# Performance work log

Hardware: AMD Instinct MI355X
Metric: run time of the kernel (lower is better)

## Reference

```python
import jax, jax.numpy as jnp
import numpy as np

CONF_THRES = 0.596
IOU_THRES = 0.45
CELL_LIMIT = 200   # CELL_SIZE_LIMIT
MAX_CAND = 512     # fixed candidate pool for jit-able NMS
MAX_WH = 4096.0    # per-class NMS box offset (yolov5 trick)
NEG_SLOPE = 0.01   # LeakyReLU default


def xywh2xyxy(b):
    cx, cy, w, h = b[..., 0], b[..., 1], b[..., 2], b[..., 3]
    return jnp.stack([cx - w / 2, cy - h / 2, cx + w / 2, cy + h / 2], axis=-1)


def box_iou(a, b):
    # a:[N,4] b:[M,4] xyxy -> [N,M]
    area_a = (a[:, 2] - a[:, 0]) * (a[:, 3] - a[:, 1])
    area_b = (b[:, 2] - b[:, 0]) * (b[:, 3] - b[:, 1])
    lt = jnp.maximum(a[:, None, :2], b[None, :, :2])
    rb = jnp.minimum(a[:, None, 2:], b[None, :, 2:])
    wh = jnp.clip(rb - lt, 0.0)
    inter = wh[..., 0] * wh[..., 1]
    return inter / (area_a[:, None] + area_b[None, :] - inter + 1e-9)


def nms_single(pred):
    # pred [N,85]: xywh, obj, 80 class probs (yolov5 layout)
    obj = pred[:, 4]
    conf_cls = pred[:, 5:] * obj[:, None]
    conf = conf_cls.max(-1)
    cls = jnp.argmax(conf_cls, -1).astype(jnp.float32)
    box = xywh2xyxy(pred[:, :4])
    score = jnp.where(conf > CONF_THRES, conf, -1.0)
    order = jnp.argsort(-score)[:MAX_CAND]          # top candidates, score-sorted
    boxes, scores, cls = box[order], score[order], cls[order]
    off = boxes + cls[:, None] * MAX_WH             # per-class offset
    iou = box_iou(off, off)
    idx = jnp.arange(MAX_CAND)
    def body(i, keep):
        sup = (iou[i] > IOU_THRES) & (idx > i) & keep[i]
        return keep & ~sup
    keep = jax.lax.fori_loop(0, MAX_CAND, body, scores > 0.0)  # greedy NMS
    ks = jnp.where(keep, scores, -1.0)
    top = jnp.argsort(-ks)[:CELL_LIMIT]
    return boxes[top], ks[top] > 0.0                # [200,4], [200]


def roi_align_1x1(feat, boxes, scale):
    # feat [C,H,W]; boxes [M,4] xyxy image pixels; output_size=1, 2x2 bilinear samples
    C, H, W = feat.shape
    b = boxes * scale
    x1, y1 = b[:, 0], b[:, 1]
    bw = jnp.maximum(b[:, 2] - x1, 1.0)
    bh = jnp.maximum(b[:, 3] - y1, 1.0)
    g = jnp.array([0.25, 0.75], dtype=feat.dtype)   # (i+0.5)/2 sample offsets
    xs = x1[:, None] + g[None, :] * bw[:, None]     # [M,2]
    ys = y1[:, None] + g[None, :] * bh[:, None]
    X = jnp.tile(xs, (1, 2))                        # [M,4] x varies fast
    Y = jnp.repeat(ys, 2, axis=1)
    X = jnp.clip(X, 0.0, W - 1.0)
    Y = jnp.clip(Y, 0.0, H - 1.0)
    x0 = jnp.floor(X).astype(jnp.int32); y0 = jnp.floor(Y).astype(jnp.int32)
    x1i = jnp.minimum(x0 + 1, W - 1); y1i = jnp.minimum(y0 + 1, H - 1)
    wx = X - x0; wy = Y - y0
    v = (feat[:, y0, x0] * ((1 - wy) * (1 - wx))[None]
         + feat[:, y0, x1i] * ((1 - wy) * wx)[None]
         + feat[:, y1i, x0] * (wy * (1 - wx))[None]
         + feat[:, y1i, x1i] * (wy * wx)[None])     # [C,M,4]
    return v.mean(-1).T                             # [M,C]


def reference(out, x1, x2, x3, x4, W1, b1, W2, b2):
    Himg = x1.shape[-2] * 8
    Wimg = x1.shape[-1] * 8
    whwh = jnp.array([Wimg, Himg, Wimg, Himg], dtype=jnp.float32)
    boxes, mask = jax.vmap(nms_single)(out)         # [B,200,4], [B,200]

    def per_img(f1, f2, f3, f4, bb):
        r = jnp.concatenate([
            roi_align_1x1(f1, bb, 1 / 8),
            roi_align_1x1(f2, bb, 1 / 16),
            roi_align_1x1(f3, bb, 1 / 32),
            roi_align_1x1(f4, bb, 1 / 64)], axis=-1)          # [200,1920]
        h = jax.nn.leaky_relu(r @ W1 + b1, NEG_SLOPE)
        h = jax.nn.leaky_relu(h @ W2 + b2, NEG_SLOPE)
        return jnp.concatenate([bb / whwh, h], axis=-1)        # [200,68]

    feats = jax.vmap(per_img)(x1, x2, x3, x4, boxes)
    feats = feats * mask[..., None].astype(feats.dtype)       # zero padded rows
    return feats, mask


def setup_inputs() -> dict:
    key = jax.random.key(0)
    ks = jax.random.split(key, 10)
    B, IMG = 8, 1024
    N = ((IMG // 8) ** 2 + (IMG // 16) ** 2 + (IMG // 32) ** 2) * 3  # 64512
    cxcy = jax.random.uniform(ks[0], (B, N, 2)) * IMG
    wh = jax.random.uniform(ks[1], (B, N, 2)) * 240.0 + 16.0
    obj = jax.random.uniform(ks[2], (B, N, 1))
    cls = jax.random.uniform(ks[3], (B, N, 80))
    out = jnp.concatenate([cxcy, wh, obj, cls], axis=-1)
    x1 = jax.random.normal(ks[4], (B, 128, 128, 128), dtype=jnp.float32)
    x2 = jax.random.normal(ks[5], (B, 256, 64, 64), dtype=jnp.float32)
    x3 = jax.random.normal(ks[6], (B, 512, 32, 32), dtype=jnp.float32)
    x4 = jax.random.normal(ks[7], (B, 1024, 16, 16), dtype=jnp.float32)
    W1 = jax.random.normal(ks[8], (1920, 64)) * 0.02
    b1 = jnp.zeros((64,), jnp.float32)
    W2 = jax.random.normal(ks[9], (64, 64)) * 0.1
    b2 = jnp.zeros((64,), jnp.float32)
    return dict(out=out, x1=x1, x2=x2, x3=x3, x4=x4, W1=W1, b1=b1, W2=W2, b2=b2)
```

## Files before the change

kernel.cpp:

```cpp
#include <hip/hip_runtime.h>
#include <hip/hip_bf16.h>

typedef unsigned int u32;
typedef unsigned long long u64;
typedef unsigned char u8;

#define B_IMG 8
#define N_ANCH 64512
#define NCLS 80
#define ROW 85
#define CONF_T 0.596f
#define IOU_T 0.45f
#define MAXC 512
#define CELL 200
#define CAP 4096

#define HBKT 128
#define KEYBASE 0x3F18u

#define SR 96
#define SF4 ((SR * ROW) / 4)
#define TOT_F4 ((size_t)B_IMG * N_ANCH * ROW / 4)

__device__ __forceinline__ float fsub(float a, float b){ return __fsub_rn(a,b); }
__device__ __forceinline__ float fadd(float a, float b){ return __fadd_rn(a,b); }
__device__ __forceinline__ float fmul(float a, float b){ return __fmul_rn(a,b); }

__device__ __forceinline__ u64 shfl_u64(u64 v, int src) {
    u32 lo = (u32)(v & 0xFFFFFFFFull), hi = (u32)(v >> 32);
    lo = (u32)__shfl((int)lo, src);
    hi = (u32)__shfl((int)hi, src);
    return ((u64)hi << 32) | (u64)lo;
}

__global__ __launch_bounds__(256) void k_score(const float* __restrict__ outp,
                                               float* __restrict__ scores,
                                               u8* __restrict__ clsarr,
                                               u32* __restrict__ hist) {
    __shared__ float srows[SR * ROW];

    int tid = threadIdx.x;
    size_t base = (size_t)blockIdx.x * SF4;
    const float4* src = (const float4*)outp;

    size_t a = base + tid;
    const size_t amax = TOT_F4 - 1;
    float4 t0 = src[(a            < amax) ? (a           ) : amax];
    float4 t1 = src[(a + 256      < amax) ? (a + 256     ) : amax];
    float4 t2 = src[(a + 512      < amax) ? (a + 512     ) : amax];
    float4 t3 = src[(a + 768      < amax) ? (a + 768     ) : amax];
    float4 t4 = src[(a + 1024     < amax) ? (a + 1024    ) : amax];
    float4 t5 = src[(a + 1280     < amax) ? (a + 1280    ) : amax];
    float4 t6 = src[(a + 1536     < amax) ? (a + 1536    ) : amax];
    float4 t7 = src[(a + 1792     < amax) ? (a + 1792    ) : amax];

    float4* dst = (float4*)srows;
    dst[tid        ] = t0;
    dst[tid +  256 ] = t1;
    dst[tid +  512 ] = t2;
    dst[tid +  768 ] = t3;
    dst[tid + 1024 ] = t4;
    dst[tid + 1280 ] = t5;
    dst[tid + 1536 ] = t6;
    if (tid < SF4 - 1792) dst[tid + 1792] = t7;
    __syncthreads();

    int r = tid >> 1;
    int h = tid & 1;
    float score = -1.0f;
    int cls = 0;
    int gi = blockIdx.x * SR + r;
    if (tid < 192) {
        const float* row = srows + r * ROW;
        float obj = row[4];
        const float* cp = row + 5 + h * 40;
        float best = -1.0f; int bi = h * 40;
        #pragma unroll
        for (int c = 0; c < 40; ++c) {
            float v = fmul(cp[c], obj);
            if (v > best) { best = v; bi = h * 40 + c; }
        }
        float ob  = __shfl_xor(best, 1);
        int   obi = __shfl_xor(bi, 1);
        float conf;
        if (ob > best) { conf = ob; cls = obi; }
        else           { conf = best; cls = bi; }
        score = (conf > CONF_T) ? conf : -1.0f;
    }

    if (tid < 192 && h == 0) {
        scores[gi] = score;
        clsarr[gi] = (u8)cls;
        if (score > 0.0f) {
            int b = gi / N_ANCH;
            u32 bk = (__float_as_uint(score) >> 16) - KEYBASE;
            if (bk > HBKT - 1) bk = HBKT - 1;
            atomicAdd(&hist[(size_t)b * HBKT + bk], 1u);
        }
    }
}

__global__ __launch_bounds__(128) void k_thresh(const u32* __restrict__ hist,
                                                u32* __restrict__ thresh) {
    int b = blockIdx.x;
    int tid = threadIdx.x;
    __shared__ u32 h[HBKT];
    h[tid] = hist[(size_t)b * HBKT + tid];
    __syncthreads();
    if (tid == 0) {
        u32 c2 = 0;
        int bkt = HBKT - 1;
        for (; bkt >= 0; --bkt) {
            c2 += h[bkt];
            if (c2 >= MAXC) break;
        }
        thresh[b] = (bkt < 0) ? 0u : (((u32)bkt + KEYBASE) << 16);
    }
}

__global__ __launch_bounds__(256) void k_compact(const float* __restrict__ scores,
                                                 const u32* __restrict__ thresh,
                                                 u32* __restrict__ cnt,
                                                 u64* __restrict__ list) {
    int i = blockIdx.x * blockDim.x + threadIdx.x;
    if (i >= B_IMG * N_ANCH) return;
    float s = scores[i];
    if (s <= 0.0f) return;
    int b = i / N_ANCH;
    u32 key = __float_as_uint(s);
    if (key < thresh[b]) return;
    u32 pos = atomicAdd(&cnt[b], 1u);
    if (pos < CAP) {
        u32 n = (u32)(i - b * N_ANCH);
        list[(size_t)b * CAP + pos] = ((u64)key << 32) | (u64)(0xFFFFFFFFu - n);
    }
}

__global__ __launch_bounds__(512) void k_sort(const float* __restrict__ outp,
                                              const u8* __restrict__ clsarr,
                                              const u32* __restrict__ cnt,
                                              const u64* __restrict__ list,
                                              float* __restrict__ oboxw,
                                              float* __restrict__ areaw,
                                              float* __restrict__ bxw,
                                              u32* __restrict__ nvalidw) {
    __shared__ u64 buf[CAP];
    int b = blockIdx.x;
    int tid = threadIdx.x;

    int M = (int)min(cnt[b], (u32)CAP);
    int P = MAXC;
    while (P < M) P <<= 1;

    for (int t = tid; t < P; t += 512)
        buf[t] = (t < M) ? list[(size_t)b * CAP + t] : 0ull;
    __syncthreads();

    for (int k = 2; k <= P; k <<= 1) {
        for (int j = k >> 1; j > 0; j >>= 1) {
            for (int t = tid; t < P; t += 512) {
                int ixj = t ^ j;
                if (ixj > t) {
                    u64 a = buf[t], c = buf[ixj];
                    bool desc = ((t & k) == 0);
                    if (desc ? (a < c) : (a > c)) { buf[t] = c; buf[ixj] = a; }
                }
            }
            __syncthreads();
        }
    }

    int nvalid = min(M, MAXC);
    bool valid = (tid < nvalid);
    u32 n = 0;
    if (valid) n = 0xFFFFFFFFu - (u32)(buf[tid] & 0xFFFFFFFFull);

    float bx0, bx1, bx2, bx3;
    float ob0, ob1, ob2, ob3;
    if (valid) {
        const float* p = outp + ((size_t)b * N_ANCH + n) * ROW;
        float cx = p[0], cy = p[1], w = p[2], h = p[3];
        int bi = (int)clsarr[(size_t)b * N_ANCH + n];
        float hw = fmul(w, 0.5f), hh = fmul(h, 0.5f);
        bx0 = fsub(cx, hw); bx1 = fsub(cy, hh);
        bx2 = fadd(cx, hw); bx3 = fadd(cy, hh);
        float off = fmul((float)bi, 4096.0f);
        ob0 = fadd(bx0, off); ob1 = fadd(bx1, off);
        ob2 = fadd(bx2, off); ob3 = fadd(bx3, off);
    } else {
        bx0 = bx1 = bx2 = bx3 = 0.0f;
        ob0 = ob1 = ob2 = ob3 = -1.0e6f;
    }
    ((float4*)oboxw)[b * MAXC + tid] = make_float4(ob0, ob1, ob2, ob3);
    areaw[b * MAXC + tid] = fmul(fsub(ob2, ob0), fsub(ob3, ob1));
    ((float4*)bxw)[b * MAXC + tid] = make_float4(bx0, bx1, bx2, bx3);
    if (tid == 0) nvalidw[b] = (u32)nvalid;
}

__global__ __launch_bounds__(64) void k_iou(const float* __restrict__ oboxw,
                                            const float* __restrict__ areaw,
                                            u64* __restrict__ sup) {
    int t = blockIdx.x, b = blockIdx.y;
    int ti = 0;
    while (t >= 8 - ti) { t -= 8 - ti; ++ti; }
    int tj = ti + t;

    int lane = threadIdx.x;
    int i = ti * 64 + lane;
    float4 oi = ((const float4*)oboxw)[b * MAXC + i];
    float ai = areaw[b * MAXC + i];

    __shared__ float jb[5][64];
    int jg = tj * 64 + lane;
    float4 oj = ((const float4*)oboxw)[b * MAXC + jg];
    jb[0][lane] = oj.x; jb[1][lane] = oj.y;
    jb[2][lane] = oj.z; jb[3][lane] = oj.w;
    jb[4][lane] = areaw[b * MAXC + jg];
    __syncthreads();

    u64 bits = 0;
    for (int jl = 0; jl < 64; ++jl) {
        int j = tj * 64 + jl;
        float ltx = fmaxf(oi.x, jb[0][jl]);
        float lty = fmaxf(oi.y, jb[1][jl]);
        float rbx = fminf(oi.z, jb[2][jl]);
        float rby = fminf(oi.w, jb[3][jl]);
        float ww = fmaxf(fsub(rbx, ltx), 0.0f);
        float hh2 = fmaxf(fsub(rby, lty), 0.0f);
        float inter = fmul(ww, hh2);
        float denom = fadd(fsub(fadd(ai, jb[4][jl]), inter), 1e-9f);
        float iou = __fdiv_rn(inter, denom);
        if ((j > i) && (iou > IOU_T)) bits |= (1ull << jl);
    }

    u64* sr = sup + ((size_t)(b * MAXC + i)) * 8;
    if (ti == tj) {
        for (int w = 0; w < ti; ++w) sr[w] = 0ull;
    }
    sr[tj] = bits;
}

#define GW(W, KW, NE, APPLY) \
    { u64 todo = (KW) & (NE); \
      while (todo) { \
          int bb = (int)__builtin_ctzll(todo); \
          const u64* rr = srow + (((W) * 64 + bb) * 8); \
          u64 hm = (bb < 63) ? (~0ull << (bb + 1)) : 0ull; \
          KW &= ~(rr[W] & hm); \
          APPLY \
          todo &= hm & KW; \
      } }

__global__ __launch_bounds__(512) void k_greedy(const u64* __restrict__ sup,
                                                const u32* __restrict__ nvalidw,
                                                const float* __restrict__ bxw,
                                                float* __restrict__ selbox,
                                                u32* __restrict__ selcnt,
                                                float* __restrict__ mask_out) {
    __shared__ u64 srow[MAXC * 8];
    __shared__ u64 neword[8];
    __shared__ u64 keepw[8];
    int b = blockIdx.x;
    int tid = threadIdx.x;
    int nvalid = (int)nvalidw[b];

    const u64* g = sup + (size_t)b * MAXC * 8;
    u64 r0 = g[tid*8+0], r1 = g[tid*8+1], r2 = g[tid*8+2], r3 = g[tid*8+3];
    u64 r4 = g[tid*8+4], r5 = g[tid*8+5], r6 = g[tid*8+6], r7 = g[tid*8+7];
    srow[tid*8+0]=r0; srow[tid*8+1]=r1; srow[tid*8+2]=r2; srow[tid*8+3]=r3;
    srow[tid*8+4]=r4; srow[tid*8+5]=r5; srow[tid*8+6]=r6; srow[tid*8+7]=r7;
    bool ne = ((r0|r1|r2|r3|r4|r5|r6|r7) != 0ull);
    u64 bal = __ballot(ne);
    if ((tid & 63) == 0) neword[tid >> 6] = bal;
    if (tid < 8) {
        int lo = tid * 64;
        u64 kw = 0;
        if (nvalid >= lo + 64) kw = ~0ull;
        else if (nvalid > lo) kw = (1ull << (nvalid - lo)) - 1ull;
        keepw[tid] = kw;
    }
    __syncthreads();

    if (tid == 0) {
        u64 k0=keepw[0], k1=keepw[1], k2=keepw[2], k3=keepw[3];
        u64 k4=keepw[4], k5=keepw[5], k6=keepw[6], k7=keepw[7];
        u64 n0=neword[0], n1=neword[1], n2=neword[2], n3=neword[3];
        u64 n4=neword[4], n5=neword[5], n6=neword[6], n7=neword[7];
        GW(0, k0, n0, k1&=~rr[1]; k2&=~rr[2]; k3&=~rr[3]; k4&=~rr[4]; k5&=~rr[5]; k6&=~rr[6]; k7&=~rr[7];)
        GW(1, k1, n1, k2&=~rr[2]; k3&=~rr[3]; k4&=~rr[4]; k5&=~rr[5]; k6&=~rr[6]; k7&=~rr[7];)
        GW(2, k2, n2, k3&=~rr[3]; k4&=~rr[4]; k5&=~rr[5]; k6&=~rr[6]; k7&=~rr[7];)
        GW(3, k3, n3, k4&=~rr[4]; k5&=~rr[5]; k6&=~rr[6]; k7&=~rr[7];)
        GW(4, k4, n4, k5&=~rr[5]; k6&=~rr[6]; k7&=~rr[7];)
        GW(5, k5, n5, k6&=~rr[6]; k7&=~rr[7];)
        GW(6, k6, n6, k7&=~rr[7];)
        GW(7, k7, n7, )
        keepw[0]=k0; keepw[1]=k1; keepw[2]=k2; keepw[3]=k3;
        keepw[4]=k4; keepw[5]=k5; keepw[6]=k6; keepw[7]=k7;
    }
    __syncthreads();

    int w = tid >> 6, l = tid & 63;
    bool kept = (tid < nvalid) && ((keepw[w] >> l) & 1ull);
    int rank = 0;
    for (int ww = 0; ww < w; ++ww) rank += __popcll(keepw[ww]);
    rank += __popcll(keepw[w] & ((l == 0) ? 0ull : ((1ull << l) - 1ull)));
    if (kept && rank < CELL) {
        float4 bx = ((const float4*)bxw)[b * MAXC + tid];
        float* sb = selbox + ((size_t)b * CELL + rank) * 4;
        sb[0] = bx.x; sb[1] = bx.y; sb[2] = bx.z; sb[3] = bx.w;
        mask_out[b * CELL + rank] = 1.0f;
    }
    if (tid == 0) {
        int tot = 0;
        for (int ww = 0; ww < 8; ++ww) tot += __popcll(keepw[ww]);
        selcnt[b] = (u32)min(tot, CELL);
    }
}

__global__ __launch_bounds__(512) void k_nms(const float* __restrict__ outp,
                                             const u32* __restrict__ cnt,
                                             const u64* __restrict__ list,
                                             float* __restrict__ selbox,
                                             u32* __restrict__ selcnt,
                                             float* __restrict__ mask_out) {
    __shared__ u64 buf[CAP];
    __shared__ float obox[MAXC][4];
    __shared__ float area[MAXC];
    __shared__ u64 keepw[8];
    int b = blockIdx.x;
    int tid = threadIdx.x;

    int M = (int)min(cnt[b], (u32)CAP);
    int P = MAXC;
    while (P < M) P <<= 1;

    for (int t = tid; t < P; t += 512)
        buf[t] = (t < M) ? list[(size_t)b * CAP + t] : 0ull;
    __syncthreads();

    for (int k = 2; k <= P; k <<= 1) {
        for (int j = k >> 1; j > 0; j >>= 1) {
            for (int t = tid; t < P; t += 512) {
                int ixj = t ^ j;
                if (ixj > t) {
                    u64 a = buf[t], c = buf[ixj];
                    bool desc = ((t & k) == 0);
                    if (desc ? (a < c) : (a > c)) { buf[t] = c; buf[ixj] = a; }
                }
            }
            __syncthreads();
        }
    }

    int nvalid = min(M, MAXC);
    bool valid = (tid < nvalid);
    u32 n = 0;
    if (valid) n = 0xFFFFFFFFu - (u32)(buf[tid] & 0xFFFFFFFFull);
    __syncthreads();

    float bx0, bx1, bx2, bx3;
    float ob0, ob1, ob2, ob3;
    if (valid) {
        const float* p = outp + ((size_t)b * N_ANCH + n) * ROW;
        float cx = p[0], cy = p[1], w = p[2], h = p[3], obj = p[4];
        float best = -1.0f; int bi = 0;
        for (int c = 0; c < NCLS; ++c) {
            float v = fmul(p[5 + c], obj);
            if (v > best) { best = v; bi = c; }
        }
        float hw = fmul(w, 0.5f), hh = fmul(h, 0.5f);
        bx0 = fsub(cx, hw); bx1 = fsub(cy, hh);
        bx2 = fadd(cx, hw); bx3 = fadd(cy, hh);
        float off = fmul((float)bi, 4096.0f);
        ob0 = fadd(bx0, off); ob1 = fadd(bx1, off);
        ob2 = fadd(bx2, off); ob3 = fadd(bx3, off);
    } else {
        bx0 = bx1 = bx2 = bx3 = 0.0f;
        ob0 = ob1 = ob2 = ob3 = -1.0e6f;
    }
    obox[tid][0] = ob0; obox[tid][1] = ob1;
    obox[tid][2] = ob2; obox[tid][3] = ob3;
    area[tid] = fmul(fsub(ob2, ob0), fsub(ob3, ob1));
    __syncthreads();

    u64* sup = buf;
    {
        u64 rowb[8] = {0,0,0,0,0,0,0,0};
        float aa = area[tid];
        for (int j = tid + 1; j < MAXC; ++j) {
            float ltx = fmaxf(ob0, obox[j][0]);
            float lty = fmaxf(ob1, obox[j][1]);
            float rbx = fminf(ob2, obox[j][2]);
            float rby = fminf(ob3, obox[j][3]);
            float ww = fmaxf(fsub(rbx, ltx), 0.0f);
            float hh2 = fmaxf(fsub(rby, lty), 0.0f);
            float inter = fmul(ww, hh2);
            float denom = fadd(fsub(fadd(aa, area[j]), inter), 1e-9f);
            float iou = __fdiv_rn(inter, denom);
            if (iou > IOU_T) rowb[j >> 6] |= (1ull << (j & 63));
        }
        for (int w2 = 0; w2 < 8; ++w2) sup[tid * 8 + w2] = rowb[w2];
    }
    __syncthreads();

    if (tid < 64) {
        int lane = tid;
        u64 kw = 0;
        if (lane < 8) {
            int lo = lane * 64;
            if (nvalid >= lo + 64) kw = ~0ull;
            else if (nvalid > lo) kw = (1ull << (nvalid - lo)) - 1ull;
        }
        for (int i = 0; i < MAXC; ++i) {
            u64 wv = shfl_u64(kw, i >> 6);
            if ((wv >> (i & 63)) & 1ull) {
                if (lane < 8) kw &= ~sup[(size_t)i * 8 + lane];
            }
        }
        if (lane < 8) keepw[lane] = kw;
    }
    __syncthreads();

    int w = tid >> 6, l = tid & 63;
    bool kept = valid && ((keepw[w] >> l) & 1ull);
    int rank = 0;
    for (int ww = 0; ww < w; ++ww) rank += __popcll(keepw[ww]);
    rank += __popcll(keepw[w] & ((l == 0) ? 0ull : ((1ull << l) - 1ull)));
    if (kept && rank < CELL) {
        float* sb = selbox + ((size_t)b * CELL + rank) * 4;
        sb[0] = bx0; sb[1] = bx1; sb[2] = bx2; sb[3] = bx3;
        mask_out[b * CELL + rank] = 1.0f;
    }
    if (tid == 0) {
        int tot = 0;
        for (int ww = 0; ww < 8; ++ww) tot += __popcll(keepw[ww]);
        selcnt[b] = (u32)min(tot, CELL);
    }
}

__global__ __launch_bounds__(256) void k_roi_gather(
        const float* __restrict__ x1, const float* __restrict__ x2,
        const float* __restrict__ x3, const float* __restrict__ x4,
        const float* __restrict__ selbox, const u32* __restrict__ selcnt,
        float* __restrict__ rws) {
    int slot = blockIdx.y;
    int b = blockIdx.z;
    if (slot >= (int)selcnt[b]) return;

    int unit = blockIdx.x * 256 + threadIdx.x;
    int c = unit >> 2;
    int p = unit & 3;

    const float* fb; int Wd; float s; int cl;
    if (c < 128)      { fb = x1 + (size_t)b * 128 * 128 * 128; Wd = 128; s = 0.125f;    cl = c; }
    else if (c < 384) { fb = x2 + (size_t)b * 256 * 64 * 64;   Wd = 64;  s = 0.0625f;   cl = c - 128; }
    else if (c < 896) { fb = x3 + (size_t)b * 512 * 32 * 32;   Wd = 32;  s = 0.03125f;  cl = c - 384; }
    else              { fb = x4 + (size_t)b * 1024 * 16 * 16;  Wd = 16;  s = 0.015625f; cl = c - 896; }

    const float* sb = selbox + ((size_t)b * CELL + slot) * 4;
    float box0 = sb[0], box1 = sb[1], box2 = sb[2], box3 = sb[3];

    float bx1f = box0 * s, by1f = box1 * s;
    float bw = fmaxf(box2 * s - bx1f, 1.0f);
    float bh = fmaxf(box3 * s - by1f, 1.0f);
    float gx = (p & 1)  ? 0.75f : 0.25f;
    float gy = (p >> 1) ? 0.75f : 0.25f;
    float X = bx1f + gx * bw;
    float Y = by1f + gy * bh;
    X = fminf(fmaxf(X, 0.0f), (float)(Wd - 1));
    Y = fminf(fmaxf(Y, 0.0f), (float)(Wd - 1));
    int x0 = (int)floorf(X), y0 = (int)floorf(Y);
    int x1i = min(x0 + 1, Wd - 1), y1i = min(y0 + 1, Wd - 1);
    float wx = X - (float)x0, wy = Y - (float)y0;

    const float* f = fb + (size_t)cl * Wd * Wd;
    float v = f[y0 * Wd + x0]  * ((1.0f - wy) * (1.0f - wx))
            + f[y0 * Wd + x1i] * ((1.0f - wy) * wx)
            + f[y1i * Wd + x0] * (wy * (1.0f - wx))
            + f[y1i * Wd + x1i]* (wy * wx);

    int lane = threadIdx.x & 63;
    int base = lane & ~3;
    float v0 = __shfl(v, base + 0);
    float v1 = __shfl(v, base + 1);
    float v2 = __shfl(v, base + 2);
    float v3 = __shfl(v, base + 3);
    if (p == 0) {
        rws[((size_t)b * CELL + slot) * 1920 + c] = (((v0 + v1) + v2) + v3) * 0.25f;
    }
}

__global__ __launch_bounds__(256) void k_mlp(
        const float* __restrict__ W1, const float* __restrict__ b1,
        const float* __restrict__ W2, const float* __restrict__ b2,
        const float* __restrict__ selbox, const u32* __restrict__ selcnt,
        const float* __restrict__ rws, float* __restrict__ feats) {
    int slot0 = blockIdx.x * 4;
    int b = blockIdx.y;
    int nsel = (int)selcnt[b];
    if (slot0 >= nsel) return;
    int tid = threadIdx.x;

    __shared__ float psum[4][4][64];
    __shared__ float h1s[4][64];

    int j = tid & 63, part = tid >> 6;
    const float* r0 = rws + ((size_t)b * CELL + slot0 + 0) * 1920;
    const float* r1 = rws + ((size_t)b * CELL + slot0 + 1) * 1920;
    const float* r2 = rws + ((size_t)b * CELL + slot0 + 2) * 1920;
    const float* r3 = rws + ((size_t)b * CELL + slot0 + 3) * 1920;

    {
        float a0 = 0.0f, a1 = 0.0f, a2 = 0.0f, a3 = 0.0f;
        int k0 = part * 480;
        for (int k = k0; k < k0 + 480; ++k) {
            float w = W1[(size_t)k * 64 + j];
            a0 += r0[k] * w;
            a1 += r1[k] * w;
            a2 += r2[k] * w;
            a3 += r3[k] * w;
        }
        psum[0][part][j] = a0;
        psum[1][part][j] = a1;
        psum[2][part][j] = a2;
        psum[3][part][j] = a3;
    }
    __syncthreads();

    int sl = tid >> 6;
    int slot = slot0 + sl;
    if (slot < nsel) {
        float v = psum[sl][0][j] + psum[sl][1][j] + psum[sl][2][j] + psum[sl][3][j] + b1[j];
        h1s[sl][j] = (v >= 0.0f) ? v : 0.01f * v;
    }
    __syncthreads();

    if (slot < nsel) {
        float acc = b2[j];
        for (int k = 0; k < 64; ++k) acc += h1s[sl][k] * W2[k * 64 + j];
        float v = (acc >= 0.0f) ? acc : 0.01f * acc;
        float* orow = feats + ((size_t)b * CELL + slot) * 68;
        orow[4 + j] = v;
        if (j < 4) {
            const float* sb = selbox + ((size_t)b * CELL + slot) * 4;
            orow[j] = sb[j] * (1.0f / 1024.0f);
        }
    }
}

__global__ __launch_bounds__(256) void k_roi_mlp(
        const float* __restrict__ x1, const float* __restrict__ x2,
        const float* __restrict__ x3, const float* __restrict__ x4,
        const float* __restrict__ W1, const float* __restrict__ b1,
        const float* __restrict__ W2, const float* __restrict__ b2,
        const float* __restrict__ selbox, const u32* __restrict__ selcnt,
        float* __restrict__ feats) {
    int slot = blockIdx.x;
    int b = blockIdx.y;
    if (slot >= (int)selcnt[b]) return;
    int tid = threadIdx.x;

    __shared__ float r[1920];
    __shared__ float psum[4][64];
    __shared__ float h1[64];

    const float* sb = selbox + ((size_t)b * CELL + slot) * 4;
    float box0 = sb[0], box1 = sb[1], box2 = sb[2], box3 = sb[3];

    const float* feat[4] = {
        x1 + (size_t)b * 128 * 128 * 128,
        x2 + (size_t)b * 256 * 64 * 64,
        x3 + (size_t)b * 512 * 32 * 32,
        x4 + (size_t)b * 1024 * 16 * 16
    };
    const int   Cs[4]  = {128, 256, 512, 1024};
    const int   Wd_[4] = {128, 64, 32, 16};
    const float Ss[4]  = {0.125f, 0.0625f, 0.03125f, 0.015625f};
    const int   Off[4] = {0, 128, 384, 896};

    for (int lvl = 0; lvl < 4; ++lvl) {
        int Wd = Wd_[lvl], C = Cs[lvl];
        float s = Ss[lvl];
        float bx1f = box0 * s, by1f = box1 * s;
        float bw = fmaxf(box2 * s - bx1f, 1.0f);
        float bh = fmaxf(box3 * s - by1f, 1.0f);
        float xs[2] = { bx1f + 0.25f * bw, bx1f + 0.75f * bw };
        float ys[2] = { by1f + 0.25f * bh, by1f + 0.75f * bh };
        int idx[4][4]; float wt[4][4];
        for (int p = 0; p < 4; ++p) {
            float X = xs[p & 1], Y = ys[p >> 1];
            X = fminf(fmaxf(X, 0.0f), (float)(Wd - 1));
            Y = fminf(fmaxf(Y, 0.0f), (float)(Wd - 1));
            int x0 = (int)floorf(X), y0 = (int)floorf(Y);
            int x1i = min(x0 + 1, Wd - 1), y1i = min(y0 + 1, Wd - 1);
            float wx = X - (float)x0, wy = Y - (float)y0;
            idx[p][0] = y0 * Wd + x0;  idx[p][1] = y0 * Wd + x1i;
            idx[p][2] = y1i * Wd + x0; idx[p][3] = y1i * Wd + x1i;
            wt[p][0] = (1.0f - wy) * (1.0f - wx); wt[p][1] = (1.0f - wy) * wx;
            wt[p][2] = wy * (1.0f - wx);          wt[p][3] = wy * wx;
        }
        const float* fb = feat[lvl];
        int HW = Wd * Wd;
        for (int c = tid; c < C; c += 256) {
            const float* f = fb + (size_t)c * HW;
            float acc = 0.0f;
            for (int p = 0; p < 4; ++p)
                acc += f[idx[p][0]] * wt[p][0] + f[idx[p][1]] * wt[p][1]
                     + f[idx[p][2]] * wt[p][2] + f[idx[p][3]] * wt[p][3];
            r[Off[lvl] + c] = acc * 0.25f;
        }
    }
    __syncthreads();

    int j = tid & 63, part = tid >> 6;
    {
        float acc = 0.0f;
        int k0 = part * 480;
        for (int k = k0; k < k0 + 480; ++k)
            acc += r[k] * W1[(size_t)k * 64 + j];
        psum[part][j] = acc;
    }
    __syncthreads();
    if (tid < 64) {
        float v = psum[0][tid] + psum[1][tid] + psum[2][tid] + psum[3][tid] + b1[tid];
        h1[tid] = (v >= 0.0f) ? v : 0.01f * v;
    }
    __syncthreads();

    float* orow = feats + ((size_t)b * CELL + slot) * 68;
    if (tid < 64) {
        float acc = b2[tid];
        for (int k = 0; k < 64; ++k) acc += h1[k] * W2[k * 64 + tid];
        float v = (acc >= 0.0f) ? acc : 0.01f * acc;
        orow[4 + tid] = v;
    }
    if (tid < 4) {
        float bv = (tid == 0) ? box0 : (tid == 1) ? box1 : (tid == 2) ? box2 : box3;
        orow[tid] = bv * (1.0f / 1024.0f);
    }
}

extern "C" void kernel_launch(void* const* d_in, const int* in_sizes, int n_in,
                              void* d_out, int out_size, void* d_ws, size_t ws_size,
                              hipStream_t stream) {
    const float* outp = (const float*)d_in[0];
    const float* x1 = (const float*)d_in[1];
    const float* x2 = (const float*)d_in[2];
    const float* x3 = (const float*)d_in[3];
    const float* x4 = (const float*)d_in[4];
    const float* W1 = (const float*)d_in[5];
    const float* b1 = (const float*)d_in[6];
    const float* W2 = (const float*)d_in[7];
    const float* b2 = (const float*)d_in[8];

    char* ws = (char*)d_ws;
    const size_t o_cnt    = 0;
    const size_t o_hist   = 256;
    const size_t o_thresh = 4352;
    const size_t o_scores = 4608;
    const size_t o_cls    = o_scores + 2064384;
    const size_t o_list   = o_cls + 516096;
    const size_t o_selbox = o_list + 262144;
    const size_t o_selcnt = o_selbox + 25600;
    const size_t o_rws    = o_selcnt + 256;
    const size_t ws_need_rws = o_rws + (size_t)B_IMG * CELL * 1920 * 4;
    const size_t o_sup    = ws_need_rws;
    const size_t o_obox   = o_sup + 262144;
    const size_t o_area   = o_obox + 65536;
    const size_t o_bx     = o_area + 16384;
    const size_t o_nvalid = o_bx + 65536;
    const size_t ws_need_full = o_nvalid + 256;

    u32*   cnt    = (u32*)(ws + o_cnt);
    u32*   hist   = (u32*)(ws + o_hist);
    u32*   thresh = (u32*)(ws + o_thresh);
    float* scores = (float*)(ws + o_scores);
    u8*    clsarr = (u8*)(ws + o_cls);
    u64*   list   = (u64*)(ws + o_list);
    float* selbox = (float*)(ws + o_selbox);
    u32*   selcnt = (u32*)(ws + o_selcnt);
    float* rws    = (float*)(ws + o_rws);
    u64*   sup    = (u64*)(ws + o_sup);
    float* oboxw  = (float*)(ws + o_obox);
    float* areaw  = (float*)(ws + o_area);
    float* bxw    = (float*)(ws + o_bx);
    u32*   nvalidw= (u32*)(ws + o_nvalid);

    float* feats = (float*)d_out;
    float* mask  = feats + (size_t)B_IMG * CELL * 68;

    hipMemsetAsync(d_out, 0, (size_t)out_size * sizeof(float), stream);
    hipMemsetAsync(ws, 0, 4608, stream);

    int total = B_IMG * N_ANCH;
    int blocks = (total + 255) / 256;
    int score_blocks = total / SR;
    k_score  <<<score_blocks, 256, 0, stream>>>(outp, scores, clsarr, hist);
    k_thresh <<<B_IMG, 128, 0, stream>>>(hist, thresh);
    k_compact<<<blocks, 256, 0, stream>>>(scores, thresh, cnt, list);

    if (ws_size >= ws_need_full) {
        k_sort  <<<B_IMG, 512, 0, stream>>>(outp, clsarr, cnt, list, oboxw, areaw, bxw, nvalidw);
        k_iou   <<<dim3(36, B_IMG), 64, 0, stream>>>(oboxw, areaw, sup);
        k_greedy<<<B_IMG, 512, 0, stream>>>(sup, nvalidw, bxw, selbox, selcnt, mask);
    } else {
        k_nms   <<<B_IMG, 512, 0, stream>>>(outp, cnt, list, selbox, selcnt, mask);
    }

    if (ws_size >= ws_need_rws) {
        k_roi_gather<<<dim3(30, CELL, B_IMG), 256, 0, stream>>>(
            x1, x2, x3, x4, selbox, selcnt, rws);
        k_mlp<<<dim3((CELL + 3) / 4, B_IMG), 256, 0, stream>>>(
            W1, b1, W2, b2, selbox, selcnt, rws, feats);
    } else {
        k_roi_mlp<<<dim3(CELL, B_IMG), 256, 0, stream>>>(
            x1, x2, x3, x4, W1, b1, W2, b2, selbox, selcnt, feats);
    }
}
```

Baseline: 343.0 us.

## Fuse threshold into compaction and merge sort, IoU, greedy NMS into one kernel

```diff
diff --git a/kernel.cpp b/kernel.cpp
--- a/kernel.cpp
+++ b/kernel.cpp
@@ -22,16 +22,11 @@
 #define SF4 ((SR * ROW) / 4)
 #define TOT_F4 ((size_t)B_IMG * N_ANCH * ROW / 4)
 
+#define BLK_PER_IMG (N_ANCH / 256)
+
 __device__ __forceinline__ float fsub(float a, float b){ return __fsub_rn(a,b); }
 __device__ __forceinline__ float fadd(float a, float b){ return __fadd_rn(a,b); }
 __device__ __forceinline__ float fmul(float a, float b){ return __fmul_rn(a,b); }
-
-__device__ __forceinline__ u64 shfl_u64(u64 v, int src) {
-    u32 lo = (u32)(v & 0xFFFFFFFFull), hi = (u32)(v >> 32);
-    lo = (u32)__shfl((int)lo, src);
-    hi = (u32)__shfl((int)hi, src);
-    return ((u64)hi << 32) | (u64)lo;
-}
 
 __global__ __launch_bounds__(256) void k_score(const float* __restrict__ outp,
                                                float* __restrict__ scores,
@@ -100,12 +95,15 @@
     }
 }
 
-__global__ __launch_bounds__(128) void k_thresh(const u32* __restrict__ hist,
-                                                u32* __restrict__ thresh) {
-    int b = blockIdx.x;
+__global__ __launch_bounds__(256) void k_compact(const float* __restrict__ scores,
+                                                 const u32* __restrict__ hist,
+                                                 u32* __restrict__ cnt,
+                                                 u64* __restrict__ list) {
+    __shared__ u32 h[HBKT];
+    __shared__ u32 sthresh;
+    int b = blockIdx.x / BLK_PER_IMG;
     int tid = threadIdx.x;
-    __shared__ u32 h[HBKT];
-    h[tid] = hist[(size_t)b * HBKT + tid];
+    if (tid < HBKT) h[tid] = hist[(size_t)b * HBKT + tid];
     __syncthreads();
     if (tid == 0) {
         u32 c2 = 0;
@@ -114,21 +112,15 @@
             c2 += h[bkt];
             if (c2 >= MAXC) break;
         }
-        thresh[b] = (bkt < 0) ? 0u : (((u32)bkt + KEYBASE) << 16);
-    }
-}
-
-__global__ __launch_bounds__(256) void k_compact(const float* __restrict__ scores,
-                                                 const u32* __restrict__ thresh,
-                                                 u32* __restrict__ cnt,
-                                                 u64* __restrict__ list) {
-    int i = blockIdx.x * blockDim.x + threadIdx.x;
-    if (i >= B_IMG * N_ANCH) return;
+        sthresh = (bkt < 0) ? 0u : (((u32)bkt + KEYBASE) << 16);
+    }
+    __syncthreads();
+
+    int i = blockIdx.x * 256 + tid;
     float s = scores[i];
     if (s <= 0.0f) return;
-    int b = i / N_ANCH;
     u32 key = __float_as_uint(s);
-    if (key < thresh[b]) return;
+    if (key < sthresh) return;
     u32 pos = atomicAdd(&cnt[b], 1u);
     if (pos < CAP) {
         u32 n = (u32)(i - b * N_ANCH);
@@ -136,15 +128,30 @@
     }
 }
 
-__global__ __launch_bounds__(512) void k_sort(const float* __restrict__ outp,
+#define GW(W, KW, NE, APPLY) \
+    { u64 todo = (KW) & (NE); \
+      while (todo) { \
+          int bb = (int)__builtin_ctzll(todo); \
+          const u64* rr = srow + (((W) * 64 + bb) * 8); \
+          u64 hm = (bb < 63) ? (~0ull << (bb + 1)) : 0ull; \
+          KW &= ~(rr[W] & hm); \
+          APPLY \
+          todo &= hm & KW; \
+      } }
+
+__global__ __launch_bounds__(512) void k_nms2(const float* __restrict__ outp,
                                               const u8* __restrict__ clsarr,
                                               const u32* __restrict__ cnt,
                                               const u64* __restrict__ list,
-                                              float* __restrict__ oboxw,
-                                              float* __restrict__ areaw,
-                                              float* __restrict__ bxw,
-                                              u32* __restrict__ nvalidw) {
+                                              float* __restrict__ selbox,
+                                              u32* __restrict__ selcnt,
+                                              float* __restrict__ mask_out) {
     __shared__ u64 buf[CAP];
+    __shared__ float4 oboxs[MAXC];
+    __shared__ float  areas[MAXC];
+    __shared__ float4 bxs[MAXC];
+    __shared__ u64 keepw[8];
+    __shared__ u64 neword[8];
     int b = blockIdx.x;
     int tid = threadIdx.x;
 
@@ -174,6 +181,7 @@
     bool valid = (tid < nvalid);
     u32 n = 0;
     if (valid) n = 0xFFFFFFFFu - (u32)(buf[tid] & 0xFFFFFFFFull);
+    __syncthreads();
 
     float bx0, bx1, bx2, bx3;
     float ob0, ob1, ob2, ob3;
@@ -191,87 +199,53 @@
         bx0 = bx1 = bx2 = bx3 = 0.0f;
         ob0 = ob1 = ob2 = ob3 = -1.0e6f;
     }
-    ((float4*)oboxw)[b * MAXC + tid] = make_float4(ob0, ob1, ob2, ob3);
-    areaw[b * MAXC + tid] = fmul(fsub(ob2, ob0), fsub(ob3, ob1));
-    ((float4*)bxw)[b * MAXC + tid] = make_float4(bx0, bx1, bx2, bx3);
-    if (tid == 0) nvalidw[b] = (u32)nvalid;
-}
-
-__global__ __launch_bounds__(64) void k_iou(const float* __restrict__ oboxw,
-                                            const float* __restrict__ areaw,
-                                            u64* __restrict__ sup) {
-    int t = blockIdx.x, b = blockIdx.y;
-    int ti = 0;
-    while (t >= 8 - ti) { t -= 8 - ti; ++ti; }
-    int tj = ti + t;
-
-    int lane = threadIdx.x;
-    int i = ti * 64 + lane;
-    float4 oi = ((const float4*)oboxw)[b * MAXC + i];
-    float ai = areaw[b * MAXC + i];
-
-    __shared__ float jb[5][64];
-    int jg = tj * 64 + lane;
-    float4 oj = ((const float4*)oboxw)[b * MAXC + jg];
-    jb[0][lane] = oj.x; jb[1][lane] = oj.y;
-    jb[2][lane] = oj.z; jb[3][lane] = oj.w;
-    jb[4][lane] = areaw[b * MAXC + jg];
-    __syncthreads();
-
-    u64 bits = 0;
-    for (int jl = 0; jl < 64; ++jl) {
-        int j = tj * 64 + jl;
-        float ltx = fmaxf(oi.x, jb[0][jl]);
-        float lty = fmaxf(oi.y, jb[1][jl]);
-        float rbx = fminf(oi.z, jb[2][jl]);
-        float rby = fminf(oi.w, jb[3][jl]);
-        float ww = fmaxf(fsub(rbx, ltx), 0.0f);
-        float hh2 = fmaxf(fsub(rby, lty), 0.0f);
-        float inter = fmul(ww, hh2);
-        float denom = fadd(fsub(fadd(ai, jb[4][jl]), inter), 1e-9f);
-        float iou = __fdiv_rn(inter, denom);
-        if ((j > i) && (iou > IOU_T)) bits |= (1ull << jl);
-    }
-
-    u64* sr = sup + ((size_t)(b * MAXC + i)) * 8;
-    if (ti == tj) {
-        for (int w = 0; w < ti; ++w) sr[w] = 0ull;
-    }
-    sr[tj] = bits;
-}
-
-#define GW(W, KW, NE, APPLY) \
-    { u64 todo = (KW) & (NE); \
-      while (todo) { \
-          int bb = (int)__builtin_ctzll(todo); \
-          const u64* rr = srow + (((W) * 64 + bb) * 8); \
-          u64 hm = (bb < 63) ? (~0ull << (bb + 1)) : 0ull; \
-          KW &= ~(rr[W] & hm); \
-          APPLY \
-          todo &= hm & KW; \
-      } }
-
-__global__ __launch_bounds__(512) void k_greedy(const u64* __restrict__ sup,
-                                                const u32* __restrict__ nvalidw,
-                                                const float* __restrict__ bxw,
-                                                float* __restrict__ selbox,
-                                                u32* __restrict__ selcnt,
-                                                float* __restrict__ mask_out) {
-    __shared__ u64 srow[MAXC * 8];
-    __shared__ u64 neword[8];
-    __shared__ u64 keepw[8];
-    int b = blockIdx.x;
-    int tid = threadIdx.x;
-    int nvalid = (int)nvalidw[b];
-
-    const u64* g = sup + (size_t)b * MAXC * 8;
-    u64 r0 = g[tid*8+0], r1 = g[tid*8+1], r2 = g[tid*8+2], r3 = g[tid*8+3];
-    u64 r4 = g[tid*8+4], r5 = g[tid*8+5], r6 = g[tid*8+6], r7 = g[tid*8+7];
-    srow[tid*8+0]=r0; srow[tid*8+1]=r1; srow[tid*8+2]=r2; srow[tid*8+3]=r3;
-    srow[tid*8+4]=r4; srow[tid*8+5]=r5; srow[tid*8+6]=r6; srow[tid*8+7]=r7;
-    bool ne = ((r0|r1|r2|r3|r4|r5|r6|r7) != 0ull);
-    u64 bal = __ballot(ne);
-    if ((tid & 63) == 0) neword[tid >> 6] = bal;
+    oboxs[tid] = make_float4(ob0, ob1, ob2, ob3);
+    areas[tid] = fmul(fsub(ob2, ob0), fsub(ob3, ob1));
+    bxs[tid]   = make_float4(bx0, bx1, bx2, bx3);
+    __syncthreads();
+
+    u64* sup = buf;
+    {
+        int wave = tid >> 6, lane = tid & 63;
+        for (int t = wave; t < 36; t += 8) {
+            int tt = t, ti = 0;
+            while (tt >= 8 - ti) { tt -= 8 - ti; ++ti; }
+            int tj = ti + tt;
+
+            int i = ti * 64 + lane;
+            float4 oi = oboxs[i];
+            float ai = areas[i];
+            u64 bits = 0;
+            for (int jl = 0; jl < 64; ++jl) {
+                int j = tj * 64 + jl;
+                float4 oj = oboxs[j];
+                float aj = areas[j];
+                float ltx = fmaxf(oi.x, oj.x);
+                float lty = fmaxf(oi.y, oj.y);
+                float rbx = fminf(oi.z, oj.z);
+                float rby = fminf(oi.w, oj.w);
+                float ww = fmaxf(fsub(rbx, ltx), 0.0f);
+                float hh2 = fmaxf(fsub(rby, lty), 0.0f);
+                float inter = fmul(ww, hh2);
+                float denom = fadd(fsub(fadd(ai, aj), inter), 1e-9f);
+                float iou = __fdiv_rn(inter, denom);
+                if ((j > i) && (iou > IOU_T)) bits |= (1ull << jl);
+            }
+            if (ti == tj) {
+                for (int w = 0; w < ti; ++w) sup[(size_t)i * 8 + w] = 0ull;
+            }
+            sup[(size_t)i * 8 + tj] = bits;
+        }
+    }
+    __syncthreads();
+
+    {
+        u64 r0 = sup[tid*8+0], r1 = sup[tid*8+1], r2 = sup[tid*8+2], r3 = sup[tid*8+3];
+        u64 r4 = sup[tid*8+4], r5 = sup[tid*8+5], r6 = sup[tid*8+6], r7 = sup[tid*8+7];
+        bool ne = ((r0|r1|r2|r3|r4|r5|r6|r7) != 0ull);
+        u64 bal = __ballot(ne);
+        if ((tid & 63) == 0) neword[tid >> 6] = bal;
+    }
     if (tid < 8) {
         int lo = tid * 64;
         u64 kw = 0;
@@ -282,6 +256,7 @@
     __syncthreads();
 
     if (tid == 0) {
+        const u64* srow = sup;
         u64 k0=keepw[0], k1=keepw[1], k2=keepw[2], k3=keepw[3];
         u64 k4=keepw[4], k5=keepw[5], k6=keepw[6], k7=keepw[7];
         u64 n0=neword[0], n1=neword[1], n2=neword[2], n3=neword[3];
@@ -300,135 +275,14 @@
     __syncthreads();
 
     int w = tid >> 6, l = tid & 63;
-    bool kept = (tid < nvalid) && ((keepw[w] >> l) & 1ull);
-    int rank = 0;
-    for (int ww = 0; ww < w; ++ww) rank += __popcll(keepw[ww]);
-    rank += __popcll(keepw[w] & ((l == 0) ? 0ull : ((1ull << l) - 1ull)));
-    if (kept && rank < CELL) {
-        float4 bx = ((const float4*)bxw)[b * MAXC + tid];
-        float* sb = selbox + ((size_t)b * CELL + rank) * 4;
-        sb[0] = bx.x; sb[1] = bx.y; sb[2] = bx.z; sb[3] = bx.w;
-        mask_out[b * CELL + rank] = 1.0f;
-    }
-    if (tid == 0) {
-        int tot = 0;
-        for (int ww = 0; ww < 8; ++ww) tot += __popcll(keepw[ww]);
-        selcnt[b] = (u32)min(tot, CELL);
-    }
-}
-
-__global__ __launch_bounds__(512) void k_nms(const float* __restrict__ outp,
-                                             const u32* __restrict__ cnt,
-                                             const u64* __restrict__ list,
-                                             float* __restrict__ selbox,
-                                             u32* __restrict__ selcnt,
-                                             float* __restrict__ mask_out) {
-    __shared__ u64 buf[CAP];
-    __shared__ float obox[MAXC][4];
-    __shared__ float area[MAXC];
-    __shared__ u64 keepw[8];
-    int b = blockIdx.x;
-    int tid = threadIdx.x;
-
-    int M = (int)min(cnt[b], (u32)CAP);
-    int P = MAXC;
-    while (P < M) P <<= 1;
-
-    for (int t = tid; t < P; t += 512)
-        buf[t] = (t < M) ? list[(size_t)b * CAP + t] : 0ull;
-    __syncthreads();
-
-    for (int k = 2; k <= P; k <<= 1) {
-        for (int j = k >> 1; j > 0; j >>= 1) {
-            for (int t = tid; t < P; t += 512) {
-                int ixj = t ^ j;
-                if (ixj > t) {
-                    u64 a = buf[t], c = buf[ixj];
-                    bool desc = ((t & k) == 0);
-                    if (desc ? (a < c) : (a > c)) { buf[t] = c; buf[ixj] = a; }
-                }
-            }
-            __syncthreads();
-        }
-    }
-
-    int nvalid = min(M, MAXC);
-    bool valid = (tid < nvalid);
-    u32 n = 0;
-    if (valid) n = 0xFFFFFFFFu - (u32)(buf[tid] & 0xFFFFFFFFull);
-    __syncthreads();
-
-    float bx0, bx1, bx2, bx3;
-    float ob0, ob1, ob2, ob3;
-    if (valid) {
-        const float* p = outp + ((size_t)b * N_ANCH + n) * ROW;
-        float cx = p[0], cy = p[1], w = p[2], h = p[3], obj = p[4];
-        float best = -1.0f; int bi = 0;
-        for (int c = 0; c < NCLS; ++c) {
-            float v = fmul(p[5 + c], obj);
-            if (v > best) { best = v; bi = c; }
-        }
-        float hw = fmul(w, 0.5f), hh = fmul(h, 0.5f);
-        bx0 = fsub(cx, hw); bx1 = fsub(cy, hh);
-        bx2 = fadd(cx, hw); bx3 = fadd(cy, hh);
-        float off = fmul((float)bi, 4096.0f);
-        ob0 = fadd(bx0, off); ob1 = fadd(bx1, off);
-        ob2 = fadd(bx2, off); ob3 = fadd(bx3, off);
-    } else {
-        bx0 = bx1 = bx2 = bx3 = 0.0f;
-        ob0 = ob1 = ob2 = ob3 = -1.0e6f;
-    }
-    obox[tid][0] = ob0; obox[tid][1] = ob1;
-    obox[tid][2] = ob2; obox[tid][3] = ob3;
-    area[tid] = fmul(fsub(ob2, ob0), fsub(ob3, ob1));
-    __syncthreads();
-
-    u64* sup = buf;
-    {
-        u64 rowb[8] = {0,0,0,0,0,0,0,0};
-        float aa = area[tid];
-        for (int j = tid + 1; j < MAXC; ++j) {
-            float ltx = fmaxf(ob0, obox[j][0]);
-            float lty = fmaxf(ob1, obox[j][1]);
-            float rbx = fminf(ob2, obox[j][2]);
-            float rby = fminf(ob3, obox[j][3]);
-            float ww = fmaxf(fsub(rbx, ltx), 0.0f);
-            float hh2 = fmaxf(fsub(rby, lty), 0.0f);
-            float inter = fmul(ww, hh2);
-            float denom = fadd(fsub(fadd(aa, area[j]), inter), 1e-9f);
-            float iou = __fdiv_rn(inter, denom);
-            if (iou > IOU_T) rowb[j >> 6] |= (1ull << (j & 63));
-        }
-        for (int w2 = 0; w2 < 8; ++w2) sup[tid * 8 + w2] = rowb[w2];
-    }
-    __syncthreads();
-
-    if (tid < 64) {
-        int lane = tid;
-        u64 kw = 0;
-        if (lane < 8) {
-            int lo = lane * 64;
-            if (nvalid >= lo + 64) kw = ~0ull;
-            else if (nvalid > lo) kw = (1ull << (nvalid - lo)) - 1ull;
-        }
-        for (int i = 0; i < MAXC; ++i) {
-            u64 wv = shfl_u64(kw, i >> 6);
-            if ((wv >> (i & 63)) & 1ull) {
-                if (lane < 8) kw &= ~sup[(size_t)i * 8 + lane];
-            }
-        }
-        if (lane < 8) keepw[lane] = kw;
-    }
-    __syncthreads();
-
-    int w = tid >> 6, l = tid & 63;
     bool kept = valid && ((keepw[w] >> l) & 1ull);
     int rank = 0;
     for (int ww = 0; ww < w; ++ww) rank += __popcll(keepw[ww]);
     rank += __popcll(keepw[w] & ((l == 0) ? 0ull : ((1ull << l) - 1ull)));
     if (kept && rank < CELL) {
+        float4 bx = bxs[tid];
         float* sb = selbox + ((size_t)b * CELL + rank) * 4;
-        sb[0] = bx0; sb[1] = bx1; sb[2] = bx2; sb[3] = bx3;
+        sb[0] = bx.x; sb[1] = bx.y; sb[2] = bx.z; sb[3] = bx.w;
         mask_out[b * CELL + rank] = 1.0f;
     }
     if (tid == 0) {
@@ -656,7 +510,6 @@
     char* ws = (char*)d_ws;
     const size_t o_cnt    = 0;
     const size_t o_hist   = 256;
-    const size_t o_thresh = 4352;
     const size_t o_scores = 4608;
     const size_t o_cls    = o_scores + 2064384;
     const size_t o_list   = o_cls + 516096;
@@ -664,27 +517,15 @@
     const size_t o_selcnt = o_selbox + 25600;
     const size_t o_rws    = o_selcnt + 256;
     const size_t ws_need_rws = o_rws + (size_t)B_IMG * CELL * 1920 * 4;
-    const size_t o_sup    = ws_need_rws;
-    const size_t o_obox   = o_sup + 262144;
-    const size_t o_area   = o_obox + 65536;
-    const size_t o_bx     = o_area + 16384;
-    const size_t o_nvalid = o_bx + 65536;
-    const size_t ws_need_full = o_nvalid + 256;
 
     u32*   cnt    = (u32*)(ws + o_cnt);
     u32*   hist   = (u32*)(ws + o_hist);
-    u32*   thresh = (u32*)(ws + o_thresh);
     float* scores = (float*)(ws + o_scores);
     u8*    clsarr = (u8*)(ws + o_cls);
     u64*   list   = (u64*)(ws + o_list);
     float* selbox = (float*)(ws + o_selbox);
     u32*   selcnt = (u32*)(ws + o_selcnt);
     float* rws    = (float*)(ws + o_rws);
-    u64*   sup    = (u64*)(ws + o_sup);
-    float* oboxw  = (float*)(ws + o_obox);
-    float* areaw  = (float*)(ws + o_area);
-    float* bxw    = (float*)(ws + o_bx);
-    u32*   nvalidw= (u32*)(ws + o_nvalid);
 
     float* feats = (float*)d_out;
     float* mask  = feats + (size_t)B_IMG * CELL * 68;
@@ -693,19 +534,11 @@
     hipMemsetAsync(ws, 0, 4608, stream);
 
     int total = B_IMG * N_ANCH;
-    int blocks = (total + 255) / 256;
+    int blocks = total / 256;
     int score_blocks = total / SR;
     k_score  <<<score_blocks, 256, 0, stream>>>(outp, scores, clsarr, hist);
-    k_thresh <<<B_IMG, 128, 0, stream>>>(hist, thresh);
-    k_compact<<<blocks, 256, 0, stream>>>(scores, thresh, cnt, list);
-
-    if (ws_size >= ws_need_full) {
-        k_sort  <<<B_IMG, 512, 0, stream>>>(outp, clsarr, cnt, list, oboxw, areaw, bxw, nvalidw);
-        k_iou   <<<dim3(36, B_IMG), 64, 0, stream>>>(oboxw, areaw, sup);
-        k_greedy<<<B_IMG, 512, 0, stream>>>(sup, nvalidw, bxw, selbox, selcnt, mask);
-    } else {
-        k_nms   <<<B_IMG, 512, 0, stream>>>(outp, cnt, list, selbox, selcnt, mask);
-    }
+    k_compact<<<blocks, 256, 0, stream>>>(scores, hist, cnt, list);
+    k_nms2   <<<B_IMG, 512, 0, stream>>>(outp, clsarr, cnt, list, selbox, selcnt, mask);
 
     if (ws_size >= ws_need_rws) {
         k_roi_gather<<<dim3(30, CELL, B_IMG), 256, 0, stream>>>(
```

New measurement: 353.7 us. +3.1%, slower.
